# Optimization experiments

Hardware: AMD Instinct MI355X
Metric: run time of the kernel (lower is better)

The kernel has to match this reference:

```python
import jax, jax.numpy as jnp
import numpy as np

N = 50000   # nodes
R = 50      # relations
B = 30      # bases
F_IN = 64   # input features
H = 64      # hidden channels
C = 8       # classes
E = 1000000 # edges


def setup_inputs() -> dict:
    key = jax.random.key(0)
    ks = jax.random.split(key, 16)
    x = jax.random.normal(ks[0], (N, F_IN), jnp.float32)
    edge_index = jax.random.randint(ks[1], (2, E), 0, N)
    edge_type = jax.random.randint(ks[2], (E,), 0, R)
    inp = {"x": x, "edge_index": edge_index, "edge_type": edge_type}
    dims = [(F_IN, H), (H, H), (H, C)]
    i = 3
    for l, (din, dout) in enumerate(dims):
        s = 1.0 / np.sqrt(din)
        inp[f"bases{l}"] = jax.random.normal(ks[i], (B, din, dout), jnp.float32) * s; i += 1
        inp[f"comp{l}"] = jax.random.normal(ks[i], (R, B), jnp.float32) / np.sqrt(B); i += 1
        inp[f"root{l}"] = jax.random.normal(ks[i], (din, dout), jnp.float32) * s; i += 1
        inp[f"bias{l}"] = jnp.zeros((dout,), jnp.float32); i += 1
    return inp


def _rgcn(x, bases, comp, root, bias, src, seg):
    # Per-relation mean aggregation (PyG RGCNConv default aggr='mean'):
    # segment id = dst * R + relation. Mean of source features per (dst, rel),
    # then basis-decomposed transform (linearity lets transform follow the mean).
    din = x.shape[1]
    sums = jax.ops.segment_sum(x[src], seg, num_segments=N * R)          # [N*R, din]
    cnt = jax.ops.segment_sum(jnp.ones((seg.shape[0],), x.dtype), seg, num_segments=N * R)
    inv = jnp.where(cnt > 0, 1.0 / jnp.maximum(cnt, 1.0), 0.0)
    agg = (sums * inv[:, None]).reshape(N, R, din)                        # [N, R, din]
    t = jnp.einsum('nri,rb->nbi', agg, comp)                              # [N, B, din]
    msg = jnp.einsum('nbi,bio->no', t, bases)                             # [N, dout]
    return msg + x @ root + bias


def reference(x, edge_index, edge_type,
              bases0, comp0, root0, bias0,
              bases1, comp1, root1, bias1,
              bases2, comp2, root2, bias2):
    src, dst = edge_index[0], edge_index[1]
    seg = dst * R + edge_type
    params = [(bases0, comp0, root0, bias0),
              (bases1, comp1, root1, bias1),
              (bases2, comp2, root2, bias2)]
    x1 = x
    for b, c, r, bi in params:
        x1 = _rgcn(x, b, c, r, bi, src, seg)
        x = jax.nn.relu(x1)
    # original returns log_softmax of the last conv's pre-ReLU output
    return jax.nn.log_softmax(x1, axis=1)
```

## Files before the change

kernel.cpp:

```cpp
#include <hip/hip_runtime.h>
#include <hip/hip_bf16.h>
#include <stdint.h>

#define NN   50000
#define RR   50
#define BB   30
#define DIN  64
#define EE   1000000
#define KTOT (BB*DIN + DIN)
#define NBW  16
#define TROW 2000

typedef __attribute__((ext_vector_type(8)))  short short8;
typedef __attribute__((ext_vector_type(4)))  float floatx4;
typedef __attribute__((ext_vector_type(16))) float floatx16;

#define RFL(x) __builtin_amdgcn_readfirstlane(x)

__device__ __forceinline__ int imin(int a, int b) { return a < b ? a : b; }

__device__ __forceinline__ void async16(const void* g, void* l) {
    __builtin_amdgcn_global_load_lds(
        (const __attribute__((address_space(1))) unsigned int*)g,
        (__attribute__((address_space(3))) unsigned int*)l, 16, 0, 0);
}


__global__ void k_hist(const int* __restrict__ dst, const int* __restrict__ et,
                       int* __restrict__ cnt, int* __restrict__ dcount) {
    int e = blockIdx.x * 256 + threadIdx.x;
    if (e < EE) {
        int d = dst[e], r = et[e];
        atomicAdd(&cnt[d * RR + r], 1);
        atomicAdd(&dcount[d], 1);
    }
}

__global__ void k_scan1(const int* __restrict__ dcount, int* __restrict__ doff,
                        int* __restrict__ bsum) {
    __shared__ int sh[256];
    int t = threadIdx.x;
    int i = blockIdx.x * 256 + t;
    int v = (i < NN) ? dcount[i] : 0;
    sh[t] = v;
    __syncthreads();
    for (int s = 1; s < 256; s <<= 1) {
        int add = (t >= s) ? sh[t - s] : 0;
        __syncthreads();
        sh[t] += add;
        __syncthreads();
    }
    int incl = sh[t];
    if (i < NN) doff[i] = incl - v;
    if (t == 255) bsum[blockIdx.x] = incl;
}

__global__ void k_scan2(int* __restrict__ bsum, int nbv) {
    __shared__ int sh[256];
    int t = threadIdx.x;
    int v = (t < nbv) ? bsum[t] : 0;
    sh[t] = v;
    __syncthreads();
    for (int s = 1; s < 256; s <<= 1) {
        int add = (t >= s) ? sh[t - s] : 0;
        __syncthreads();
        sh[t] += add;
        __syncthreads();
    }
    if (t < nbv) bsum[t] = sh[t] - v;
}

__global__ void k_scan3(int* __restrict__ doff, const int* __restrict__ bsum) {
    int i = blockIdx.x * 256 + threadIdx.x;
    if (i < NN) doff[i] += bsum[blockIdx.x];
}

__global__ void k_scatter(const int* __restrict__ src, const int* __restrict__ dst,
                          const int* __restrict__ et, const int* __restrict__ cnt,
                          const int* __restrict__ doff, int* __restrict__ cursor,
                          int4* __restrict__ epack) {
    int e = blockIdx.x * 256 + threadIdx.x;
    if (e < EE) {
        int d = dst[e], r = et[e], s = src[e];
        int p = doff[d] + atomicAdd(&cursor[d], 1);
        float a = 1.0f / (float)cnt[d * RR + r];
        epack[p] = make_int4(s, r, __float_as_int(a), 0);
    }
}

__global__ void k_cast_x(const float* __restrict__ x, __hip_bfloat16* __restrict__ h) {
    int i = blockIdx.x * 256 + threadIdx.x;
    if (i < NN * DIN) h[i] = __float2bfloat16(x[i]);
}

__global__ void k_prep_cb3(const float* __restrict__ c0, const float* __restrict__ c1,
                           const float* __restrict__ c2, short* __restrict__ cb) {
    int idx = blockIdx.x * 256 + threadIdx.x;
    if (idx < 3 * RR * 32) {
        int l = idx / (RR * 32);
        int rem = idx - l * (RR * 32);
        int r = rem >> 5, i = rem & 31;
        const float* c = (l == 0) ? c0 : (l == 1) ? c1 : c2;
        float v = (i < BB) ? c[r * BB + i] : 0.f;
        __hip_bfloat16 hb = __float2bfloat16(v);
        cb[idx] = *reinterpret_cast<const short*>(&hb);
    }
}

__global__ void k_prep_w3(const float* __restrict__ b0, const float* __restrict__ r0,
                          const float* __restrict__ b1, const float* __restrict__ r1,
                          const float* __restrict__ b2, const float* __restrict__ r2,
                          short* __restrict__ wt) {
    int idx = blockIdx.x * 256 + threadIdx.x;
    if (idx >= 144 * KTOT) return;
    int row = idx / KTOT, k = idx - row * KTOT;
    const float* bs; const float* rt; int o, dout;
    if (row < 64)       { bs = b0; rt = r0; o = row;        dout = 64; }
    else if (row < 128) { bs = b1; rt = r1; o = row - 64;   dout = 64; }
    else                { bs = b2; rt = r2; o = row - 128;  dout = 8;  }
    float v = 0.f;
    if (o < dout)
        v = (k < BB * DIN) ? bs[k * dout + o] : rt[(k - BB * DIN) * dout + o];
    __hip_bfloat16 hb = __float2bfloat16(v);
    wt[idx] = *reinterpret_cast<const short*>(&hb);
}

template <int DOUT, bool RELU>
__global__ __launch_bounds__(1024, 4)
void k_fused(const __hip_bfloat16* __restrict__ xin,
             const int4* __restrict__ epack,
             const int* __restrict__ doff, const int* __restrict__ dcount,
             const short* __restrict__ cpb,
             const short* __restrict__ Wt,
             const float* __restrict__ bias,
             void* __restrict__ outp) {
    __shared__ __align__(16) char smem[NBW * TROW * 2];
    short* t_tile = (short*)smem;

    const int tid  = threadIdx.x;
    const int lane = tid & 63;
    const int wv   = RFL(tid >> 6);
    const int node0 = blockIdx.x * NBW;
    const int m    = lane & 31;
    const bool hi  = (lane >= 32);

    floatx16 acc0 = {0.f,0.f,0.f,0.f,0.f,0.f,0.f,0.f,0.f,0.f,0.f,0.f,0.f,0.f,0.f,0.f};
    floatx16 acc1 = acc0;
    {
        const int n = node0 + wv;
        const int beg = RFL(doff[n]), cnt = RFL(dcount[n]);
        const int nch = (cnt + 15) >> 4;
        char*  sst_b = smem + wv * 2048;
        const short* sst = (const short*)sst_b;
        const int eg  = lane >> 3;
        const int sub = (lane & 7) * 16;
        const int k0  = (lane >> 5) * 8;

        int4 vr0, vr1;
        if (nch > 0) {
            vr0 = epack[imin(beg + eg,     EE - 1)];
            vr1 = epack[imin(beg + eg + 8, EE - 1)];
        }
        for (int c = 0; c < nch; ++c) {
            const int cb = beg + c * 16;
            const char* g0 = (const char*)xin + ((size_t)(unsigned)vr0.x) * 128 + sub;
            const char* g1 = (const char*)xin + ((size_t)(unsigned)vr1.x) * 128 + sub;
            async16(g0, sst_b);
            async16(g1, sst_b + 1024);
            if (c + 1 < nch) {
                const int nb = cb + 16;
                vr0 = epack[imin(nb + eg,     EE - 1)];
                vr1 = epack[imin(nb + eg + 8, EE - 1)];
            }
            int relA[8], relB[8]; float alA[8], alB[8];
#pragma unroll
            for (int t = 0; t < 8; ++t) {
                int4 ea = epack[imin(cb + t,     EE - 1)];
                int4 eb = epack[imin(cb + 8 + t, EE - 1)];
                relA[t] = ea.y;
                relB[t] = eb.y;
                alA[t] = (c * 16 + t     < cnt) ? __int_as_float(ea.z) : 0.f;
                alB[t] = (c * 16 + 8 + t < cnt) ? __int_as_float(eb.z) : 0.f;
            }
            short8 af;
#pragma unroll
            for (int t = 0; t < 8; ++t) {
                int   rel = hi ? relB[t] : relA[t];
                float al  = hi ? alB[t]  : alA[t];
                unsigned short cv = ((const unsigned short*)cpb)[rel * 32 + m];
                float cf = __int_as_float(((int)cv) << 16);
                af[t] = (short)(((unsigned)__float_as_int(cf * al)) >> 16);
            }
            __builtin_amdgcn_s_waitcnt(0x0F70);
            __builtin_amdgcn_sched_barrier(0);
            short8 bf0, bf1;
#pragma unroll
            for (int t = 0; t < 8; ++t) {
                bf0[t] = sst[(k0 + t) * 64 + m];
                bf1[t] = sst[(k0 + t) * 64 + 32 + m];
            }
            acc0 = __builtin_amdgcn_mfma_f32_32x32x16_bf16(af, bf0, acc0, 0, 0, 0);
            acc1 = __builtin_amdgcn_mfma_f32_32x32x16_bf16(af, bf1, acc1, 0, 0, 0);
        }
    }
    __syncthreads();

    {
        short* trow = t_tile + wv * TROW;
#pragma unroll
        for (int r = 0; r < 16; ++r) {
            const int b = (r & 3) + 8 * (r >> 2) + 4 * (lane >> 5);
            if (b < BB) {
                __hip_bfloat16 h0 = __float2bfloat16(acc0[r]);
                __hip_bfloat16 h1 = __float2bfloat16(acc1[r]);
                trow[b * 64 + m]      = *reinterpret_cast<const short*>(&h0);
                trow[b * 64 + 32 + m] = *reinterpret_cast<const short*>(&h1);
            }
        }
        trow[BB * 64 + lane] = ((const short*)xin)[(node0 + wv) * 64 + lane];
    }
    __syncthreads();

    const int mm = lane & 15;
    const int qq = lane >> 4;
    floatx4 p0 = {0.f, 0.f, 0.f, 0.f};
    floatx4 p1 = {0.f, 0.f, 0.f, 0.f};
    int cp, kp;
    if (DOUT == 64) { cp = wv & 1; kp = wv >> 1; }
    else            { cp = 0;      kp = wv;      }
    int kk0, nst;
    if (DOUT == 64) { kk0 = (kp < 6)  ? kp * 8 : 48 + (kp - 6)  * 7; nst = (kp < 6)  ? 8 : 7; }
    else            { kk0 = (kp < 14) ? kp * 4 : 56 + (kp - 14) * 3; nst = (kp < 14) ? 4 : 3; }

    {
        const short* arow = t_tile + mm * TROW + qq * 8;
        const short* b0row = Wt + (size_t)(cp * 32 + mm) * KTOT + qq * 8;
        const short* b1row = Wt + (size_t)(cp * 32 + 16 + mm) * KTOT + qq * 8;
        for (int s = 0; s < nst; ++s) {
            const int kk = kk0 + s;
            short8 a  = *reinterpret_cast<const short8*>(arow + kk * 32);
            short8 w0 = *reinterpret_cast<const short8*>(b0row + kk * 32);
            p0 = __builtin_amdgcn_mfma_f32_16x16x32_bf16(a, w0, p0, 0, 0, 0);
            if (DOUT == 64) {
                short8 w1 = *reinterpret_cast<const short8*>(b1row + kk * 32);
                p1 = __builtin_amdgcn_mfma_f32_16x16x32_bf16(a, w1, p1, 0, 0, 0);
            }
        }
    }

    __syncthreads();
    float* red = (float*)smem;

    if (DOUT == 64) {
        if (kp > 0) {
            const int off = ((cp * 7 + (kp - 1)) * 64 + lane) * 9;
#pragma unroll
            for (int i = 0; i < 4; ++i) { red[off + i] = p0[i]; red[off + 4 + i] = p1[i]; }
        }
        __syncthreads();
        if (kp == 0) {
#pragma unroll
            for (int w = 0; w < 7; ++w) {
                const int off = ((cp * 7 + w) * 64 + lane) * 9;
#pragma unroll
                for (int i = 0; i < 4; ++i) { p0[i] += red[off + i]; p1[i] += red[off + 4 + i]; }
            }
#pragma unroll
            for (int t = 0; t < 2; ++t) {
                const int o = cp * 32 + t * 16 + mm;
                const float bi = bias[o];
                floatx4& P = t ? p1 : p0;
#pragma unroll
                for (int r = 0; r < 4; ++r) {
                    const int n = node0 + qq * 4 + r;
                    float v = P[r] + bi;
                    if (RELU) {
                        v = fmaxf(v, 0.f);
                        reinterpret_cast<__hip_bfloat16*>(outp)[(size_t)n * DOUT + o] =
                            __float2bfloat16(v);
                    } else {
                        reinterpret_cast<float*>(outp)[(size_t)n * DOUT + o] = v;
                    }
                }
            }
        }
    } else {
        if (kp > 0) {
            const int off = (((kp - 1)) * 64 + lane) * 5;
#pragma unroll
            for (int i = 0; i < 4; ++i) red[off + i] = p0[i];
        }
        __syncthreads();
        if (kp == 0) {
#pragma unroll
            for (int w = 0; w < 15; ++w) {
                const int off = (w * 64 + lane) * 5;
#pragma unroll
                for (int i = 0; i < 4; ++i) p0[i] += red[off + i];
            }
            if (mm < DOUT) {
                const float bi = bias[mm];
#pragma unroll
                for (int r = 0; r < 4; ++r) {
                    const int n = node0 + qq * 4 + r;
                    reinterpret_cast<float*>(outp)[(size_t)n * DOUT + mm] = p0[r] + bi;
                }
            }
        }
    }
}

__global__ void k_lsm(const float* __restrict__ pre, float* __restrict__ out) {
    int n = blockIdx.x * 256 + threadIdx.x;
    if (n < NN) {
        float v[8];
        float mx = -1e30f;
#pragma unroll
        for (int c = 0; c < 8; ++c) { v[c] = pre[n * 8 + c]; mx = fmaxf(mx, v[c]); }
        float s = 0.f;
#pragma unroll
        for (int c = 0; c < 8; ++c) s += expf(v[c] - mx);
        float ls = logf(s);
#pragma unroll
        for (int c = 0; c < 8; ++c) out[n * 8 + c] = v[c] - mx - ls;
    }
}

extern "C" void kernel_launch(void* const* d_in, const int* in_sizes, int n_in,
                              void* d_out, int out_size, void* d_ws, size_t ws_size,
                              hipStream_t stream) {
    const float* x     = (const float*)d_in[0];
    const int*   eidx  = (const int*)d_in[1];
    const int*   etype = (const int*)d_in[2];
    const float* bases0 = (const float*)d_in[3];
    const float* comp0  = (const float*)d_in[4];
    const float* root0  = (const float*)d_in[5];
    const float* bias0  = (const float*)d_in[6];
    const float* bases1 = (const float*)d_in[7];
    const float* comp1  = (const float*)d_in[8];
    const float* root1  = (const float*)d_in[9];
    const float* bias1  = (const float*)d_in[10];
    const float* bases2 = (const float*)d_in[11];
    const float* comp2  = (const float*)d_in[12];
    const float* root2  = (const float*)d_in[13];
    const float* bias2  = (const float*)d_in[14];
    const int* srcp = eidx;
    const int* dstp = eidx + EE;

    char* p = (char*)d_ws;
    auto carve = [&](size_t bytes) -> char* {
        char* r = p;
        p += (bytes + 255) & ~(size_t)255;
        return r;
    };
    int*  cnt    = (int*)carve((size_t)NN * RR * sizeof(int));
    int*  dcount = (int*)carve((size_t)NN * sizeof(int));
    int*  cursor = (int*)carve((size_t)NN * sizeof(int));
    int*  doff   = (int*)carve((size_t)NN * sizeof(int));
    int*  bsum   = (int*)carve(256 * sizeof(int));
    int4* epack  = (int4*)carve((size_t)EE * sizeof(int4) + 512);
    __hip_bfloat16* h0 = (__hip_bfloat16*)carve((size_t)NN * DIN * 2);
    __hip_bfloat16* h1 = (__hip_bfloat16*)carve((size_t)NN * DIN * 2);
    __hip_bfloat16* h2 = (__hip_bfloat16*)carve((size_t)NN * DIN * 2);
    float* pre = (float*)carve((size_t)NN * 8 * sizeof(float));
    short* wtA = (short*)carve((size_t)144 * KTOT * sizeof(short));
    short* cbA = (short*)carve((size_t)3 * RR * 32 * sizeof(short));

    hipMemsetAsync(cnt, 0, (size_t)NN * (RR + 2) * sizeof(int) + 512, stream);

    const int EB = (EE + 255) / 256;
    const int NB = (NN + 255) / 256;
    k_hist<<<EB, 256, 0, stream>>>(dstp, etype, cnt, dcount);
    k_scan1<<<NB, 256, 0, stream>>>(dcount, doff, bsum);
    k_scan2<<<1, 256, 0, stream>>>(bsum, NB);
    k_scan3<<<NB, 256, 0, stream>>>(doff, bsum);
    k_scatter<<<EB, 256, 0, stream>>>(srcp, dstp, etype, cnt, doff, cursor, epack);
    k_cast_x<<<(NN * DIN + 255) / 256, 256, 0, stream>>>(x, h0);
    k_prep_cb3<<<(3 * RR * 32 + 255) / 256, 256, 0, stream>>>(comp0, comp1, comp2, cbA);
    k_prep_w3<<<(144 * KTOT + 255) / 256, 256, 0, stream>>>(bases0, root0, bases1, root1,
                                                            bases2, root2, wtA);

    short* wt0 = wtA;
    short* wt1 = wtA + (size_t)64 * KTOT;
    short* wt2 = wtA + (size_t)128 * KTOT;
    short* cb0 = cbA;
    short* cb1 = cbA + RR * 32;
    short* cb2 = cbA + 2 * RR * 32;

    const int NF = NN / NBW;
    k_fused<64, true ><<<NF, 1024, 0, stream>>>(h0, epack, doff, dcount, cb0, wt0, bias0, (void*)h1);
    k_fused<64, true ><<<NF, 1024, 0, stream>>>(h1, epack, doff, dcount, cb1, wt1, bias1, (void*)h2);
    k_fused<8,  false><<<NF, 1024, 0, stream>>>(h2, epack, doff, dcount, cb2, wt2, bias2, (void*)pre);
    k_lsm<<<NB, 256, 0, stream>>>(pre, (float*)d_out);
}
```

Before: 652.2 us.

## Pad per-node edge lists to 16 and restructure fused RGCN kernel to 8 nodes per block

Edge offsets are padded to multiples of 16, with a zeroed padded edge buffer, so chunk loads need no bounds clamping or masking. Each block now handles 8 nodes, with two waves per node each covering one 32-column half. Edge records are double-buffered into LDS via async loads, and the comp table is cached in LDS. Source features are gathered directly from global into registers instead of staged through LDS. Occupancy hint rises to 8 blocks and the second GEMM is re-split across 4 column tiles, but this adds a memset of a larger epack buffer and wastes half of each 16-row MFMA tile.

```diff
diff --git a/kernel.cpp b/kernel.cpp
--- a/kernel.cpp
+++ b/kernel.cpp
@@ -7,17 +7,16 @@
 #define BB   30
 #define DIN  64
 #define EE   1000000
+#define E16MAX (EE + NN * 15)
 #define KTOT (BB*DIN + DIN)
-#define NBW  16
-#define TROW 2000
+#define NBW  8
+#define TROW8 1992
 
 typedef __attribute__((ext_vector_type(8)))  short short8;
 typedef __attribute__((ext_vector_type(4)))  float floatx4;
 typedef __attribute__((ext_vector_type(16))) float floatx16;
 
 #define RFL(x) __builtin_amdgcn_readfirstlane(x)
-
-__device__ __forceinline__ int imin(int a, int b) { return a < b ? a : b; }
 
 __device__ __forceinline__ void async16(const void* g, void* l) {
     __builtin_amdgcn_global_load_lds(
@@ -41,7 +40,7 @@
     __shared__ int sh[256];
     int t = threadIdx.x;
     int i = blockIdx.x * 256 + t;
-    int v = (i < NN) ? dcount[i] : 0;
+    int v = (i < NN) ? ((dcount[i] + 15) & ~15) : 0;
     sh[t] = v;
     __syncthreads();
     for (int s = 1; s < 256; s <<= 1) {
@@ -126,167 +125,149 @@
 }
 
 template <int DOUT, bool RELU>
-__global__ __launch_bounds__(1024, 4)
+__global__ __launch_bounds__(1024, 8)
 void k_fused(const __hip_bfloat16* __restrict__ xin,
              const int4* __restrict__ epack,
-             const int* __restrict__ doff, const int* __restrict__ dcount,
+             const int* __restrict__ doff16, const int* __restrict__ dcount,
              const short* __restrict__ cpb,
              const short* __restrict__ Wt,
              const float* __restrict__ bias,
              void* __restrict__ outp) {
-    __shared__ __align__(16) char smem[NBW * TROW * 2];
-    short* t_tile = (short*)smem;
+    __shared__ __align__(16) char smem[43264];
+    short* comp_lds = (short*)smem;
+    char*  recs     = smem + 3200;
+    short* t_tile   = (short*)(smem + 11392);
 
     const int tid  = threadIdx.x;
     const int lane = tid & 63;
     const int wv   = RFL(tid >> 6);
     const int node0 = blockIdx.x * NBW;
-    const int m    = lane & 31;
-    const bool hi  = (lane >= 32);
-
-    floatx16 acc0 = {0.f,0.f,0.f,0.f,0.f,0.f,0.f,0.f,0.f,0.f,0.f,0.f,0.f,0.f,0.f,0.f};
-    floatx16 acc1 = acc0;
+    const int j   = wv >> 1;
+    const int h   = wv & 1;
+    const int m31 = lane & 31;
+    const int kh  = lane >> 5;
+
+    for (int i = tid; i < 800; i += 1024)
+        ((int*)comp_lds)[i] = ((const int*)cpb)[i];
+    __syncthreads();
+
+    floatx16 acc = {0.f,0.f,0.f,0.f,0.f,0.f,0.f,0.f,0.f,0.f,0.f,0.f,0.f,0.f,0.f,0.f};
+    const int n   = node0 + j;
+    const int beg = RFL(doff16[n]);
+    const int nch = (RFL(dcount[n]) + 15) >> 4;
+    char* rs = recs + wv * 512;
+
+    if (nch > 0) {
+        if (lane < 16)
+            async16((const char*)epack + ((size_t)beg + lane) * 16, rs);
+        for (int c = 0; c < nch; ++c) {
+            const char* cur = rs + (c & 1) * 256;
+            char* nxt = rs + ((c + 1) & 1) * 256;
+            if (c + 1 < nch) {
+                if (lane < 16)
+                    async16((const char*)epack + ((size_t)(beg + (c + 1) * 16) + lane) * 16, nxt);
+                __builtin_amdgcn_s_waitcnt(0x0F71);
+            } else {
+                __builtin_amdgcn_s_waitcnt(0x0F70);
+            }
+            unsigned short xv[8];
+            float av[8];
+#pragma unroll
+            for (int t = 0; t < 8; ++t) {
+                int4 rc = *(const int4*)(cur + (kh * 8 + t) * 16);
+                xv[t] = *(const unsigned short*)((const char*)xin
+                          + ((size_t)(unsigned)rc.x) * 128 + h * 64 + m31 * 2);
+                unsigned short cw = *(const unsigned short*)
+                          ((const char*)comp_lds + rc.y * 64 + m31 * 2);
+                float cf = __int_as_float(((int)cw) << 16);
+                av[t] = cf * __int_as_float(rc.z);
+            }
+            short8 A, B;
+#pragma unroll
+            for (int t = 0; t < 8; ++t) {
+                __hip_bfloat16 ab = __float2bfloat16(av[t]);
+                A[t] = *reinterpret_cast<const short*>(&ab);
+                B[t] = (short)xv[t];
+            }
+            acc = __builtin_amdgcn_mfma_f32_32x32x16_bf16(A, B, acc, 0, 0, 0);
+        }
+    }
+
     {
-        const int n = node0 + wv;
-        const int beg = RFL(doff[n]), cnt = RFL(dcount[n]);
-        const int nch = (cnt + 15) >> 4;
-        char*  sst_b = smem + wv * 2048;
-        const short* sst = (const short*)sst_b;
-        const int eg  = lane >> 3;
-        const int sub = (lane & 7) * 16;
-        const int k0  = (lane >> 5) * 8;
-
-        int4 vr0, vr1;
-        if (nch > 0) {
-            vr0 = epack[imin(beg + eg,     EE - 1)];
-            vr1 = epack[imin(beg + eg + 8, EE - 1)];
-        }
-        for (int c = 0; c < nch; ++c) {
-            const int cb = beg + c * 16;
-            const char* g0 = (const char*)xin + ((size_t)(unsigned)vr0.x) * 128 + sub;
-            const char* g1 = (const char*)xin + ((size_t)(unsigned)vr1.x) * 128 + sub;
-            async16(g0, sst_b);
-            async16(g1, sst_b + 1024);
-            if (c + 1 < nch) {
-                const int nb = cb + 16;
-                vr0 = epack[imin(nb + eg,     EE - 1)];
-                vr1 = epack[imin(nb + eg + 8, EE - 1)];
-            }
-            int relA[8], relB[8]; float alA[8], alB[8];
-#pragma unroll
-            for (int t = 0; t < 8; ++t) {
-                int4 ea = epack[imin(cb + t,     EE - 1)];
-                int4 eb = epack[imin(cb + 8 + t, EE - 1)];
-                relA[t] = ea.y;
-                relB[t] = eb.y;
-                alA[t] = (c * 16 + t     < cnt) ? __int_as_float(ea.z) : 0.f;
-                alB[t] = (c * 16 + 8 + t < cnt) ? __int_as_float(eb.z) : 0.f;
-            }
-            short8 af;
-#pragma unroll
-            for (int t = 0; t < 8; ++t) {
-                int   rel = hi ? relB[t] : relA[t];
-                float al  = hi ? alB[t]  : alA[t];
-                unsigned short cv = ((const unsigned short*)cpb)[rel * 32 + m];
-                float cf = __int_as_float(((int)cv) << 16);
-                af[t] = (short)(((unsigned)__float_as_int(cf * al)) >> 16);
-            }
-            __builtin_amdgcn_s_waitcnt(0x0F70);
-            __builtin_amdgcn_sched_barrier(0);
-            short8 bf0, bf1;
-#pragma unroll
-            for (int t = 0; t < 8; ++t) {
-                bf0[t] = sst[(k0 + t) * 64 + m];
-                bf1[t] = sst[(k0 + t) * 64 + 32 + m];
-            }
-            acc0 = __builtin_amdgcn_mfma_f32_32x32x16_bf16(af, bf0, acc0, 0, 0, 0);
-            acc1 = __builtin_amdgcn_mfma_f32_32x32x16_bf16(af, bf1, acc1, 0, 0, 0);
-        }
-    }
-    __syncthreads();
-
-    {
-        short* trow = t_tile + wv * TROW;
+        short* trow = t_tile + j * TROW8;
 #pragma unroll
         for (int r = 0; r < 16; ++r) {
-            const int b = (r & 3) + 8 * (r >> 2) + 4 * (lane >> 5);
+            const int b = (r & 3) + 8 * (r >> 2) + 4 * kh;
             if (b < BB) {
-                __hip_bfloat16 h0 = __float2bfloat16(acc0[r]);
-                __hip_bfloat16 h1 = __float2bfloat16(acc1[r]);
-                trow[b * 64 + m]      = *reinterpret_cast<const short*>(&h0);
-                trow[b * 64 + 32 + m] = *reinterpret_cast<const short*>(&h1);
-            }
-        }
-        trow[BB * 64 + lane] = ((const short*)xin)[(node0 + wv) * 64 + lane];
+                __hip_bfloat16 hv = __float2bfloat16(acc[r]);
+                trow[b * 64 + h * 32 + m31] = *reinterpret_cast<const short*>(&hv);
+            }
+        }
+        trow[BB * 64 + h * 32 + m31] = ((const short*)xin)[(size_t)n * 64 + h * 32 + m31];
     }
     __syncthreads();
 
     const int mm = lane & 15;
     const int qq = lane >> 4;
+    int ct, kp, kk0, nst;
+    if (DOUT == 64) {
+        ct = wv & 3; kp = wv >> 2;
+        kk0 = (kp <= 1) ? kp * 16 : (kp == 2 ? 32 : 47);
+        nst = (kp <= 1) ? 16 : 15;
+    } else {
+        ct = 0; kp = wv;
+        kk0 = (kp < 14) ? kp * 4 : 56 + (kp - 14) * 3;
+        nst = (kp < 14) ? 4 : 3;
+    }
     floatx4 p0 = {0.f, 0.f, 0.f, 0.f};
-    floatx4 p1 = {0.f, 0.f, 0.f, 0.f};
-    int cp, kp;
-    if (DOUT == 64) { cp = wv & 1; kp = wv >> 1; }
-    else            { cp = 0;      kp = wv;      }
-    int kk0, nst;
-    if (DOUT == 64) { kk0 = (kp < 6)  ? kp * 8 : 48 + (kp - 6)  * 7; nst = (kp < 6)  ? 8 : 7; }
-    else            { kk0 = (kp < 14) ? kp * 4 : 56 + (kp - 14) * 3; nst = (kp < 14) ? 4 : 3; }
-
     {
-        const short* arow = t_tile + mm * TROW + qq * 8;
-        const short* b0row = Wt + (size_t)(cp * 32 + mm) * KTOT + qq * 8;
-        const short* b1row = Wt + (size_t)(cp * 32 + 16 + mm) * KTOT + qq * 8;
+        const short* arow = t_tile + mm * TROW8 + qq * 8;
+        const short* wrow = Wt + (size_t)(ct * 16 + mm) * KTOT + qq * 8;
         for (int s = 0; s < nst; ++s) {
             const int kk = kk0 + s;
-            short8 a  = *reinterpret_cast<const short8*>(arow + kk * 32);
-            short8 w0 = *reinterpret_cast<const short8*>(b0row + kk * 32);
-            p0 = __builtin_amdgcn_mfma_f32_16x16x32_bf16(a, w0, p0, 0, 0, 0);
-            if (DOUT == 64) {
-                short8 w1 = *reinterpret_cast<const short8*>(b1row + kk * 32);
-                p1 = __builtin_amdgcn_mfma_f32_16x16x32_bf16(a, w1, p1, 0, 0, 0);
-            }
-        }
-    }
-
+            short8 a = {0, 0, 0, 0, 0, 0, 0, 0};
+            if (mm < NBW) a = *(const short8*)(arow + kk * 32);
+            short8 w = *(const short8*)(wrow + kk * 32);
+            p0 = __builtin_amdgcn_mfma_f32_16x16x32_bf16(a, w, p0, 0, 0, 0);
+        }
+    }
     __syncthreads();
     float* red = (float*)smem;
 
     if (DOUT == 64) {
         if (kp > 0) {
-            const int off = ((cp * 7 + (kp - 1)) * 64 + lane) * 9;
-#pragma unroll
-            for (int i = 0; i < 4; ++i) { red[off + i] = p0[i]; red[off + 4 + i] = p1[i]; }
+            const int off = ((ct * 3 + (kp - 1)) * 64 + lane) * 5;
+#pragma unroll
+            for (int i = 0; i < 4; ++i) red[off + i] = p0[i];
         }
         __syncthreads();
         if (kp == 0) {
 #pragma unroll
-            for (int w = 0; w < 7; ++w) {
-                const int off = ((cp * 7 + w) * 64 + lane) * 9;
-#pragma unroll
-                for (int i = 0; i < 4; ++i) { p0[i] += red[off + i]; p1[i] += red[off + 4 + i]; }
-            }
-#pragma unroll
-            for (int t = 0; t < 2; ++t) {
-                const int o = cp * 32 + t * 16 + mm;
+            for (int w = 0; w < 3; ++w) {
+                const int off = ((ct * 3 + w) * 64 + lane) * 5;
+#pragma unroll
+                for (int i = 0; i < 4; ++i) p0[i] += red[off + i];
+            }
+            if (qq < 2) {
+                const int o = ct * 16 + mm;
                 const float bi = bias[o];
-                floatx4& P = t ? p1 : p0;
 #pragma unroll
                 for (int r = 0; r < 4; ++r) {
-                    const int n = node0 + qq * 4 + r;
-                    float v = P[r] + bi;
+                    const int nn = node0 + qq * 4 + r;
+                    float v = p0[r] + bi;
                     if (RELU) {
                         v = fmaxf(v, 0.f);
-                        reinterpret_cast<__hip_bfloat16*>(outp)[(size_t)n * DOUT + o] =
+                        reinterpret_cast<__hip_bfloat16*>(outp)[(size_t)nn * DOUT + o] =
                             __float2bfloat16(v);
                     } else {
-                        reinterpret_cast<float*>(outp)[(size_t)n * DOUT + o] = v;
+                        reinterpret_cast<float*>(outp)[(size_t)nn * DOUT + o] = v;
                     }
                 }
             }
         }
     } else {
         if (kp > 0) {
-            const int off = (((kp - 1)) * 64 + lane) * 5;
+            const int off = ((kp - 1) * 64 + lane) * 5;
 #pragma unroll
             for (int i = 0; i < 4; ++i) red[off + i] = p0[i];
         }
@@ -298,12 +279,12 @@
 #pragma unroll
                 for (int i = 0; i < 4; ++i) p0[i] += red[off + i];
             }
-            if (mm < DOUT) {
+            if (mm < DOUT && qq < 2) {
                 const float bi = bias[mm];
 #pragma unroll
                 for (int r = 0; r < 4; ++r) {
-                    const int n = node0 + qq * 4 + r;
-                    reinterpret_cast<float*>(outp)[(size_t)n * DOUT + mm] = p0[r] + bi;
+                    const int nn = node0 + qq * 4 + r;
+                    reinterpret_cast<float*>(outp)[(size_t)nn * DOUT + mm] = p0[r] + bi;
                 }
             }
         }
@@ -358,7 +339,7 @@
     int*  cursor = (int*)carve((size_t)NN * sizeof(int));
     int*  doff   = (int*)carve((size_t)NN * sizeof(int));
     int*  bsum   = (int*)carve(256 * sizeof(int));
-    int4* epack  = (int4*)carve((size_t)EE * sizeof(int4) + 512);
+    int4* epack  = (int4*)carve((size_t)E16MAX * sizeof(int4) + 512);
     __hip_bfloat16* h0 = (__hip_bfloat16*)carve((size_t)NN * DIN * 2);
     __hip_bfloat16* h1 = (__hip_bfloat16*)carve((size_t)NN * DIN * 2);
     __hip_bfloat16* h2 = (__hip_bfloat16*)carve((size_t)NN * DIN * 2);
@@ -367,6 +348,7 @@
     short* cbA = (short*)carve((size_t)3 * RR * 32 * sizeof(short));
 
     hipMemsetAsync(cnt, 0, (size_t)NN * (RR + 2) * sizeof(int) + 512, stream);
+    hipMemsetAsync(epack, 0, (size_t)E16MAX * sizeof(int4), stream);
 
     const int EB = (EE + 255) / 256;
     const int NB = (NN + 255) / 256;
```

Result: slower. 756.3 us (+16.0%).
